# Kernel optimization log

Measured on AMD Instinct MI355X. Metric: run time of the kernel, lower is better.

The kernel has to match this reference:

```python
import jax, jax.numpy as jnp
import numpy as np

R_MAX = 5.0
NUM_BASIS = 8
CUTOFF_P = 6
N_LAYERS = 3
C = 64          # hidden_mul / channels of irreps_conv_out (64x0e+64x1o)
Z = 4           # element_number
AVG_DEG = 32.0  # num-neighbor normalization (E/N)
SQRT3 = 1.7320508075688772
SQRT2 = 1.4142135623730951


def _radial_embedding(r):
    # Bessel basis * polynomial cutoff (RadialEdgeEmbedding)
    rs = jnp.maximum(r, 1e-9)
    n = jnp.arange(1, NUM_BASIS + 1, dtype=r.dtype)  # (B,)
    bessel = jnp.sqrt(2.0 / R_MAX) * jnp.sin(n * jnp.pi * rs[:, None] / R_MAX) / rs[:, None]
    x = r / R_MAX
    p = float(CUTOFF_P)
    fc = (1.0
          - (p + 1.0) * (p + 2.0) / 2.0 * x ** CUTOFF_P
          + p * (p + 2.0) * x ** (CUTOFF_P + 1)
          - p * (p + 1.0) / 2.0 * x ** (CUTOFF_P + 2))
    fc = jnp.where(x < 1.0, fc, 0.0)
    return bessel * fc[:, None]  # (E, NUM_BASIS)


def setup_inputs() -> dict:
    key = jax.random.key(0)
    ks = jax.random.split(key, 20)
    N, E, B = 16000, 512000, 16
    atom_type = jax.random.randint(ks[0], (N,), 0, Z)
    # atoms in a 4A box so most edge lengths fall inside r_max=5
    atom_pos = jax.random.uniform(ks[1], (N, 3), dtype=jnp.float32) * 4.0
    edge_src = jax.random.randint(ks[2], (E,), 0, N)
    edge_dst = jax.random.randint(ks[3], (E,), 0, N)
    edge_cell_shift = jnp.zeros((E, 3), jnp.float32)
    cell = jnp.tile(jnp.eye(3, dtype=jnp.float32) * 10.0, (B, 1, 1)) \
        + 0.01 * jax.random.normal(ks[4], (B, 3, 3), jnp.float32)
    image_index = jax.random.randint(ks[5], (N,), 0, B)
    g = lambda k, s, fan: jax.random.normal(k, s, jnp.float32) / np.sqrt(fan)
    return {
        'atom_type': atom_type, 'atom_pos': atom_pos,
        'edge_src': edge_src, 'edge_dst': edge_dst,
        'edge_cell_shift': edge_cell_shift, 'cell': cell, 'image_index': image_index,
        'w_lin_in': g(ks[6], (Z, C), Z),
        'mlp_w1': g(ks[7], (N_LAYERS, NUM_BASIS, 64), NUM_BASIS),
        'mlp_b1': jnp.zeros((N_LAYERS, 64), jnp.float32),
        'mlp_w2': g(ks[8], (N_LAYERS, 64, 5 * C), 64),
        'w_self_s': g(ks[9], (N_LAYERS, C, C), C),
        'w_self_v': g(ks[10], (N_LAYERS, C, C), C),
        'w_gate': g(ks[11], (N_LAYERS, C, C), C),
        'w_lin1': g(ks[12], (C, 16), C),
        'w_lin2': g(ks[13], (16, 1), 16),
    }


def reference(atom_type, atom_pos, edge_src, edge_dst, edge_cell_shift, cell,
              image_index, w_lin_in, mlp_w1, mlp_b1, mlp_w2,
              w_self_s, w_self_v, w_gate, w_lin1, w_lin2):
    N = atom_pos.shape[0]
    # edge vectors with periodic cell shift
    edge_vec = atom_pos[edge_dst] - atom_pos[edge_src]
    edge_vec = edge_vec + jnp.einsum('ni,nij->nj', edge_cell_shift,
                                     cell.reshape(-1, 3, 3)[image_index[edge_src]])
    r = jnp.linalg.norm(edge_vec, axis=1)                      # (E,)
    unit = edge_vec / jnp.maximum(r, 1e-9)[:, None]
    # spherical harmonics lmax=1, component normalization: y0=1 (implicit), y1=sqrt(3)*unit
    y1 = SQRT3 * unit                                           # (E, 3)
    emb = _radial_embedding(r)                                  # (E, NUM_BASIS)

    # one-hot embedding + input linear (one-hot is all 0e -> scalar channels only)
    onehot = jax.nn.one_hot(atom_type, Z, dtype=atom_pos.dtype)
    s = onehot @ w_lin_in                                       # (N, C) l=0 features
    v = jnp.zeros((N, C, 3), atom_pos.dtype)                    # (N, C, 3) l=1 features

    inv_sqrt_deg = 1.0 / np.sqrt(AVG_DEG)
    for L in range(N_LAYERS):
        # radial MLP -> per-edge per-channel tensor-product path weights
        w = jax.nn.silu(emb @ mlp_w1[L] + mlp_b1[L]) @ mlp_w2[L]  # (E, 5C)
        w1, w2, w3, w4, w5 = jnp.split(w, 5, axis=1)              # (E, C) each
        s_src = s[edge_src]                                       # (E, C)
        v_src = v[edge_src]                                       # (E, C, 3)
        vdoty = jnp.einsum('ecx,ex->ec', v_src, y1)
        # CG tensor-product paths (l<=1):
        m_s = w1 * s_src + w2 * vdoty / SQRT3                     # 0x0->0, 1x1->0
        m_v = (w3[:, :, None] * s_src[:, :, None] * y1[:, None, :]      # 0x1->1
               + w4[:, :, None] * v_src                                  # 1x0->1
               + w5[:, :, None] * jnp.cross(v_src, y1[:, None, :]) / SQRT2)  # 1x1->1
        agg_s = jax.ops.segment_sum(m_s, edge_dst, num_segments=N) * inv_sqrt_deg
        agg_v = jax.ops.segment_sum(m_v, edge_dst, num_segments=N) * inv_sqrt_deg
        # gated self-interaction + resnet
        gate = jax.nn.sigmoid(agg_s @ w_gate[L])                  # (N, C)
        s = s + jax.nn.silu(agg_s @ w_self_s[L])
        v = v + jnp.einsum('ncx,cd->ndx', agg_v, w_self_v[L]) * gate[:, :, None]

    # o3.Linear to 16x0e then 1x0e (only scalar channels map to 0e outputs)
    atomic_energy = (s @ w_lin1) @ w_lin2                         # (N, 1)
    atomic_energy = atomic_energy * 1.0                           # atomic_scale
    return atomic_energy
```

## Files before the change

kernel.cpp:

```cpp
#include <hip/hip_runtime.h>
#include <hip/hip_fp16.h>
#include <math.h>

#define NUM_BASIS 8
#define SQRT3 1.7320508075688772f
#define SQRT2 1.4142135623730951f
#define INV_SQRT_DEG 0.17677669529663687f
#define PI_F 3.14159265358979323846f

typedef _Float16 half8 __attribute__((ext_vector_type(8)));
typedef float float4v __attribute__((ext_vector_type(4)));

__device__ __forceinline__ float sigmoidf_(float x) { return 1.0f / (1.0f + __expf(-x)); }
__device__ __forceinline__ float siluf_(float x) { return x * sigmoidf_(x); }

__device__ __forceinline__ void unp2(unsigned u, float& a, float& b) {
    __half2 h = *reinterpret_cast<__half2*>(&u);
    float2 f = __half22float2(h);
    a = f.x; b = f.y;
}
__device__ __forceinline__ unsigned pk2(float a, float b) {
    __half2 h = __floats2half2_rn(a, b);
    return *reinterpret_cast<unsigned*>(&h);
}

__global__ __launch_bounds__(256) void count_deg(
    const int* __restrict__ dst, int* __restrict__ deg, int E)
{
    int base = (blockIdx.x * blockDim.x + threadIdx.x) * 4;
    if (base + 3 < E) {
        int4 d4 = *(const int4*)(dst + base);
        atomicAdd(&deg[d4.x], 1);
        atomicAdd(&deg[d4.y], 1);
        atomicAdd(&deg[d4.z], 1);
        atomicAdd(&deg[d4.w], 1);
    } else {
        for (int e = base; e < E; e++) atomicAdd(&deg[dst[e]], 1);
    }
}

__global__ __launch_bounds__(1024) void scan_deg(
    const int* __restrict__ deg, int* __restrict__ cursor, int N)
{
    __shared__ int wsum[16];
    __shared__ int carry_s, tot_s;
    int tid = threadIdx.x;
    int wid = tid >> 6, lane = tid & 63;
    if (tid == 0) carry_s = 0;
    __syncthreads();
    for (int base = 0; base < N; base += 16384) {
        int i0 = base + tid * 16;
        int v[16];
        int sum = 0;
        #pragma unroll
        for (int k = 0; k < 16; k++) {
            int i = i0 + k;
            v[k] = (i < N) ? deg[i] : 0;
            sum += v[k];
        }
        int incl = sum;
        #pragma unroll
        for (int off = 1; off < 64; off <<= 1) {
            int t = __shfl_up(incl, off);
            if (lane >= off) incl += t;
        }
        if (lane == 63) wsum[wid] = incl;
        __syncthreads();
        if (wid == 0 && lane < 16) {
            int wv = wsum[lane];
            int wincl = wv;
            #pragma unroll
            for (int off = 1; off < 16; off <<= 1) {
                int t = __shfl_up(wincl, off);
                if (lane >= off) wincl += t;
            }
            wsum[lane] = wincl - wv;
            if (lane == 15) tot_s = wincl;
        }
        __syncthreads();
        int carry = carry_s;
        int run = carry + wsum[wid] + incl - sum;
        #pragma unroll
        for (int k = 0; k < 16; k++) {
            int i = i0 + k;
            if (i < N) cursor[i] = run;
            run += v[k];
        }
        __syncthreads();
        if (tid == 0) carry_s = carry + tot_s;
        __syncthreads();
    }
}

__global__ __launch_bounds__(256) void edge_pre_scatter(
    const float* __restrict__ pos, const int* __restrict__ src,
    const int* __restrict__ dst, const float* __restrict__ cs,
    const float* __restrict__ cell, const int* __restrict__ img,
    int* __restrict__ cursor, _Float16* __restrict__ emb,
    uint2* __restrict__ y14, int2* __restrict__ sdp, int E)
{
    int e = blockIdx.x * blockDim.x + threadIdx.x;
    if (e >= E) return;
    int si = src[e], di = dst[e];
    int slot = atomicAdd(&cursor[di], 1);
    sdp[slot] = make_int2(si, di);
    float vx = pos[di*3+0] - pos[si*3+0];
    float vy = pos[di*3+1] - pos[si*3+1];
    float vz = pos[di*3+2] - pos[si*3+2];
    float c0 = cs[(size_t)e*3+0], c1 = cs[(size_t)e*3+1], c2 = cs[(size_t)e*3+2];
    const float* M = cell + (size_t)img[si] * 9;
    vx += c0*M[0] + c1*M[3] + c2*M[6];
    vy += c0*M[1] + c1*M[4] + c2*M[7];
    vz += c0*M[2] + c1*M[5] + c2*M[8];
    float r  = sqrtf(vx*vx + vy*vy + vz*vz);
    float rs = fmaxf(r, 1e-9f);
    float inv = 1.0f / rs;
    uint2 yv;
    yv.x = pk2(SQRT3*vx*inv, SQRT3*vy*inv);
    yv.y = pk2(SQRT3*vz*inv, 0.f);
    y14[slot] = yv;
    float x = r * (1.0f / 5.0f);
    float x2 = x*x, x6 = x2*x2*x2;
    float fc = 1.0f - 28.0f*x6 + 48.0f*x6*x - 21.0f*x6*x2;
    if (x >= 1.0f) fc = 0.0f;
    float pre = sqrtf(2.0f / 5.0f) * inv * fc;
    float t = PI_F * rs * (1.0f / 5.0f);
    half8 ev;
    #pragma unroll
    for (int n = 1; n <= NUM_BASIS; n++)
        ev[n-1] = (_Float16)(pre * __sinf((float)n * t));
    *(half8*)(emb + (size_t)slot*NUM_BASIS) = ev;
}

__global__ __launch_bounds__(256) void prep_weights(
    const float* __restrict__ W2, _Float16* __restrict__ w2f,
    const float* __restrict__ Wg, const float* __restrict__ Ws,
    const float* __restrict__ Wv, _Float16* __restrict__ wgtf,
    const float* __restrict__ Wl1, const float* __restrict__ Wl2,
    float* __restrict__ wl12)
{
    int idx = blockIdx.x * blockDim.x + threadIdx.x;
    if (idx < 64) {
        float a = 0.f;
        #pragma unroll
        for (int j = 0; j < 16; j++) a = fmaf(Wl1[idx*16 + j], Wl2[j], a);
        wl12[idx] = a;
    }
    if (idx < 3 * 20480) {
        int L  = idx / 20480;
        int r  = idx % 20480;
        int cg = r / 5120;
        int r2 = r % 5120;
        int p  = r2 / 1024;
        int r3 = r2 % 1024;
        int kh = r3 / 512;
        int r4 = r3 % 512;
        int lane = r4 / 8;
        int j  = r4 % 8;
        int k = kh*32 + (lane >> 4)*8 + j;
        int n = p*64 + cg*16 + (lane & 15);
        w2f[idx] = (_Float16)W2[(size_t)L*20480 + k*320 + n];
    } else if (idx < 3*20480 + 3*3*4096) {
        int idx2 = idx - 3*20480;
        int L   = idx2 / 12288;
        int rem = idx2 % 12288;
        int mat = rem / 4096;
        int r2  = rem % 4096;
        int cg  = r2 / 1024;
        int r3  = r2 % 1024;
        int kh  = r3 / 512;
        int r4  = r3 % 512;
        int lane = r4 / 8;
        int j   = r4 % 8;
        int k = kh*32 + (lane >> 4)*8 + j;
        int n = cg*16 + (lane & 15);
        const float* src = (mat == 0) ? Wg : (mat == 1) ? Ws : Wv;
        wgtf[idx2] = (_Float16)src[(size_t)L*4096 + k*64 + n];
    }
}

__device__ __forceinline__ void mlp1_afrag(
    const _Float16* __restrict__ emb, const float* __restrict__ W1,
    const float* __restrict__ B1, int eA, int q, half8 afrag[2])
{
    half8 ev = *(const half8*)(emb + (size_t)eA*8);
    float em[8];
    #pragma unroll
    for (int j = 0; j < 8; j++) em[j] = (float)ev[j];
    #pragma unroll
    for (int kh = 0; kh < 2; kh++) {
        int kb = kh*32 + q*8;
        float hv[8];
        float4 b0 = *(const float4*)(B1 + kb);
        float4 b1 = *(const float4*)(B1 + kb + 4);
        hv[0]=b0.x; hv[1]=b0.y; hv[2]=b0.z; hv[3]=b0.w;
        hv[4]=b1.x; hv[5]=b1.y; hv[6]=b1.z; hv[7]=b1.w;
        #pragma unroll
        for (int jj = 0; jj < 8; jj++) {
            float4 wa = *(const float4*)(W1 + jj*64 + kb);
            float4 wb = *(const float4*)(W1 + jj*64 + kb + 4);
            hv[0] = fmaf(em[jj], wa.x, hv[0]);
            hv[1] = fmaf(em[jj], wa.y, hv[1]);
            hv[2] = fmaf(em[jj], wa.z, hv[2]);
            hv[3] = fmaf(em[jj], wa.w, hv[3]);
            hv[4] = fmaf(em[jj], wb.x, hv[4]);
            hv[5] = fmaf(em[jj], wb.y, hv[5]);
            hv[6] = fmaf(em[jj], wb.z, hv[6]);
            hv[7] = fmaf(em[jj], wb.w, hv[7]);
        }
        #pragma unroll
        for (int j = 0; j < 8; j++)
            afrag[kh][j] = (_Float16)siluf_(hv[j]);
    }
}

__global__ __launch_bounds__(256) void edge_msg_mfma_l0(
    const _Float16* __restrict__ emb, const uint2* __restrict__ y14,
    const int2* __restrict__ sdp,
    const int* __restrict__ type, const float* __restrict__ wlin,
    const float* __restrict__ W1, const float* __restrict__ B1,
    const _Float16* __restrict__ w2f,
    float* __restrict__ aggs, float* __restrict__ aggx,
    float* __restrict__ aggy, float* __restrict__ aggz, int E)
{
    __shared__ _Float16 w2s[20480];
    {
        half8* dstv = (half8*)w2s;
        const half8* srcv = (const half8*)w2f;
        #pragma unroll
        for (int k = 0; k < 10; k++)
            dstv[threadIdx.x + k*256] = srcv[threadIdx.x + k*256];
    }
    __syncthreads();

    int wave  = (blockIdx.x * blockDim.x + threadIdx.x) >> 6;
    int lane  = threadIdx.x & 63;
    int wbase = wave * 16;
    if (wbase >= E) return;
    int q   = lane >> 4;
    int col = lane & 15;

    int eb = wbase + q*4;
    int d[4], tt[4];
    float y1x[4], y1y[4], y1z[4];
    #pragma unroll
    for (int r = 0; r < 4; r++) {
        int2 sv = sdp[eb + r];
        tt[r] = type[sv.x];
        d[r]  = sv.y;
        uint2 yv = y14[eb + r];
        float dummy;
        unp2(yv.x, y1x[r], y1y[r]);
        unp2(yv.y, y1z[r], dummy);
    }

    half8 afrag[2];
    mlp1_afrag(emb, W1, B1, wbase + col, q, afrag);

    int dnq = __shfl_down(d[0], 16);
    int nd3 = (q == 3) ? -1 : dnq;
    int df = d[0], dl = d[3];
    bool U = (df == dl);
    int dlp = __shfl_up(dl, 16);
    bool link = (q > 0) && (dlp == df);

    #pragma unroll
    for (int cg = 0; cg < 4; cg++) {
        float4v a1 = {0,0,0,0}, a3 = {0,0,0,0};
        const _Float16* wbp = w2s + ((size_t)cg*5*2*64*8) + (size_t)lane*8;
        {
            half8 b10 = *(const half8*)(wbp + ((size_t)(0*2 + 0))*64*8);
            half8 b11 = *(const half8*)(wbp + ((size_t)(0*2 + 1))*64*8);
            half8 b30 = *(const half8*)(wbp + ((size_t)(2*2 + 0))*64*8);
            half8 b31 = *(const half8*)(wbp + ((size_t)(2*2 + 1))*64*8);
            a1 = __builtin_amdgcn_mfma_f32_16x16x32_f16(afrag[0], b10, a1, 0, 0, 0);
            a1 = __builtin_amdgcn_mfma_f32_16x16x32_f16(afrag[1], b11, a1, 0, 0, 0);
            a3 = __builtin_amdgcn_mfma_f32_16x16x32_f16(afrag[0], b30, a3, 0, 0, 0);
            a3 = __builtin_amdgcn_mfma_f32_16x16x32_f16(afrag[1], b31, a3, 0, 0, 0);
        }
        int c = cg*16 + col;

        float ms[4], mx[4], my[4], mz[4];
        #pragma unroll
        for (int r = 0; r < 4; r++) {
            float s = wlin[tt[r]*64 + c];
            float w3s = a3[r] * s;
            ms[r] = a1[r] * s;
            mx[r] = w3s * y1x[r];
            my[r] = w3s * y1y[r];
            mz[r] = w3s * y1z[r];
        }
        #pragma unroll
        for (int r = 1; r < 4; r++) {
            if (d[r] == d[r-1]) {
                ms[r] += ms[r-1]; mx[r] += mx[r-1];
                my[r] += my[r-1]; mz[r] += mz[r-1];
            }
        }
        float Cs = 0.f, Cx = 0.f, Cy = 0.f, Cz = 0.f;
        #pragma unroll
        for (int it = 0; it < 3; it++) {
            float es = ms[3] + (U ? Cs : 0.f);
            float ex = mx[3] + (U ? Cx : 0.f);
            float ey = my[3] + (U ? Cy : 0.f);
            float ez = mz[3] + (U ? Cz : 0.f);
            float ts = __shfl_up(es, 16);
            float tx = __shfl_up(ex, 16);
            float ty = __shfl_up(ey, 16);
            float tz = __shfl_up(ez, 16);
            Cs = link ? ts : 0.f; Cx = link ? tx : 0.f;
            Cy = link ? ty : 0.f; Cz = link ? tz : 0.f;
        }
        bool hr = true;
        #pragma unroll
        for (int r = 0; r < 4; r++) {
            if (r > 0) hr = hr && (d[r] == d[r-1]);
            float fs = ms[r] + (hr ? Cs : 0.f);
            float fx = mx[r] + (hr ? Cx : 0.f);
            float fy = my[r] + (hr ? Cy : 0.f);
            float fz = mz[r] + (hr ? Cz : 0.f);
            int ndx = (r < 3) ? d[r+1] : nd3;
            if (ndx != d[r] && d[r] >= 0) {
                size_t ai = (size_t)d[r]*64 + c;
                atomicAdd(aggs + ai, fs);
                atomicAdd(aggx + ai, fx);
                atomicAdd(aggy + ai, fy);
                atomicAdd(aggz + ai, fz);
            }
        }
    }
}

__global__ __launch_bounds__(256) void edge_msg_mfma(
    const _Float16* __restrict__ emb, const uint2* __restrict__ y14,
    const int2* __restrict__ sdp,
    const uint2* __restrict__ nf,
    const float* __restrict__ W1, const float* __restrict__ B1,
    const _Float16* __restrict__ w2f,
    float* __restrict__ aggs, float* __restrict__ aggx,
    float* __restrict__ aggy, float* __restrict__ aggz, int E)
{
    __shared__ _Float16 w2s[20480];
    {
        half8* dstv = (half8*)w2s;
        const half8* srcv = (const half8*)w2f;
        #pragma unroll
        for (int k = 0; k < 10; k++)
            dstv[threadIdx.x + k*256] = srcv[threadIdx.x + k*256];
    }
    __syncthreads();

    int wave  = (blockIdx.x * blockDim.x + threadIdx.x) >> 6;
    int lane  = threadIdx.x & 63;
    int wbase = wave * 16;
    if (wbase >= E) return;
    int q   = lane >> 4;
    int col = lane & 15;

    int eb = wbase + q*4;
    int d[4], si[4];
    float y1x[4], y1y[4], y1z[4];
    #pragma unroll
    for (int r = 0; r < 4; r++) {
        int2 sv = sdp[eb + r];
        si[r] = sv.x;
        d[r]  = sv.y;
        uint2 yv = y14[eb + r];
        float dummy;
        unp2(yv.x, y1x[r], y1y[r]);
        unp2(yv.y, y1z[r], dummy);
    }

    uint2 pf[4][4];
    #pragma unroll
    for (int r = 0; r < 4; r++) {
        size_t nb = (size_t)si[r] * 64 + col;
        pf[r][0] = nf[nb];
        pf[r][1] = nf[nb + 16];
        pf[r][2] = nf[nb + 32];
        pf[r][3] = nf[nb + 48];
    }

    half8 afrag[2];
    mlp1_afrag(emb, W1, B1, wbase + col, q, afrag);

    int dnq = __shfl_down(d[0], 16);
    int nd3 = (q == 3) ? -1 : dnq;
    int df = d[0], dl = d[3];
    bool U = (df == dl);
    int dlp = __shfl_up(dl, 16);
    bool link = (q > 0) && (dlp == df);

    #pragma unroll
    for (int cg = 0; cg < 4; cg++) {
        float4v acc[5];
        #pragma unroll
        for (int p = 0; p < 5; p++) acc[p] = (float4v){0.f, 0.f, 0.f, 0.f};
        const _Float16* wbp = w2s + ((size_t)cg*5*2*64*8) + (size_t)lane*8;
        #pragma unroll
        for (int p = 0; p < 5; p++) {
            half8 bf0 = *(const half8*)(wbp + ((size_t)(p*2 + 0))*64*8);
            half8 bf1 = *(const half8*)(wbp + ((size_t)(p*2 + 1))*64*8);
            acc[p] = __builtin_amdgcn_mfma_f32_16x16x32_f16(afrag[0], bf0, acc[p], 0, 0, 0);
            acc[p] = __builtin_amdgcn_mfma_f32_16x16x32_f16(afrag[1], bf1, acc[p], 0, 0, 0);
        }
        int c = cg*16 + col;

        float ms[4], mx[4], my[4], mz[4];
        #pragma unroll
        for (int r = 0; r < 4; r++) {
            float fsx, fvx, fvy, fvz;
            unp2(pf[r][cg].x, fsx, fvx);
            unp2(pf[r][cg].y, fvy, fvz);
            float yx = y1x[r], yy = y1y[r], yz = y1z[r];
            float w1 = acc[0][r], w2 = acc[1][r], w3 = acc[2][r];
            float w4 = acc[3][r], w5 = acc[4][r];
            float vdoty = fvx*yx + fvy*yy + fvz*yz;
            ms[r] = w1*fsx + w2*vdoty*(1.0f/SQRT3);
            float cx = fvy*yz - fvz*yy;
            float cy = fvz*yx - fvx*yz;
            float cz = fvx*yy - fvy*yx;
            mx[r] = w3*fsx*yx + w4*fvx + w5*cx*(1.0f/SQRT2);
            my[r] = w3*fsx*yy + w4*fvy + w5*cy*(1.0f/SQRT2);
            mz[r] = w3*fsx*yz + w4*fvz + w5*cz*(1.0f/SQRT2);
        }
        #pragma unroll
        for (int r = 1; r < 4; r++) {
            if (d[r] == d[r-1]) {
                ms[r] += ms[r-1]; mx[r] += mx[r-1];
                my[r] += my[r-1]; mz[r] += mz[r-1];
            }
        }
        float Cs = 0.f, Cx = 0.f, Cy = 0.f, Cz = 0.f;
        #pragma unroll
        for (int it = 0; it < 3; it++) {
            float es = ms[3] + (U ? Cs : 0.f);
            float ex = mx[3] + (U ? Cx : 0.f);
            float ey = my[3] + (U ? Cy : 0.f);
            float ez = mz[3] + (U ? Cz : 0.f);
            float ts = __shfl_up(es, 16);
            float tx = __shfl_up(ex, 16);
            float ty = __shfl_up(ey, 16);
            float tz = __shfl_up(ez, 16);
            Cs = link ? ts : 0.f; Cx = link ? tx : 0.f;
            Cy = link ? ty : 0.f; Cz = link ? tz : 0.f;
        }
        bool hr = true;
        #pragma unroll
        for (int r = 0; r < 4; r++) {
            if (r > 0) hr = hr && (d[r] == d[r-1]);
            float fs = ms[r] + (hr ? Cs : 0.f);
            float fx = mx[r] + (hr ? Cx : 0.f);
            float fy = my[r] + (hr ? Cy : 0.f);
            float fz = mz[r] + (hr ? Cz : 0.f);
            int ndx = (r < 3) ? d[r+1] : nd3;
            if (ndx != d[r] && d[r] >= 0) {
                size_t ai = (size_t)d[r]*64 + c;
                atomicAdd(aggs + ai, fs);
                atomicAdd(aggx + ai, fx);
                atomicAdd(aggy + ai, fy);
                atomicAdd(aggz + ai, fz);
            }
        }
    }
}

__global__ __launch_bounds__(256) void node_update_mfma(
    uint2* __restrict__ nf,
    float* __restrict__ aggs, float* __restrict__ aggx,
    float* __restrict__ aggy, float* __restrict__ aggz,
    const _Float16* __restrict__ wgtf,
    const int* __restrict__ type, const float* __restrict__ wlin,
    const float* __restrict__ wl12,
    float* __restrict__ out, int first, int do_out, int N)
{
    __shared__ _Float16 wgs[12288];
    {
        half8* dstv = (half8*)wgs;
        const half8* srcv = (const half8*)wgtf;
        #pragma unroll
        for (int k = 0; k < 6; k++)
            dstv[threadIdx.x + k*256] = srcv[threadIdx.x + k*256];
    }

    int wave  = (blockIdx.x * blockDim.x + threadIdx.x) >> 6;
    int lane  = threadIdx.x & 63;
    int wbase = wave * 16;
    bool active = wbase < N;
    int q = lane >> 4, col = lane & 15;

    int nodeA = active ? (wbase + col) : 0;
    if (nodeA >= N) nodeA = N - 1;
    size_t nb = (size_t)nodeA * 64 + q * 8;
    half8 af0[2], af1[2], af2[2], af3[2];
    #pragma unroll
    for (int kh = 0; kh < 2; kh++) {
        const float* p0 = aggs + nb + kh*32;
        const float* p1 = aggx + nb + kh*32;
        const float* p2 = aggy + nb + kh*32;
        const float* p3 = aggz + nb + kh*32;
        float4 a0 = *(const float4*)p0, b0 = *(const float4*)(p0+4);
        float4 a1 = *(const float4*)p1, b1 = *(const float4*)(p1+4);
        float4 a2 = *(const float4*)p2, b2 = *(const float4*)(p2+4);
        float4 a3 = *(const float4*)p3, b3 = *(const float4*)(p3+4);
        af0[kh][0]=(_Float16)(a0.x*INV_SQRT_DEG); af0[kh][1]=(_Float16)(a0.y*INV_SQRT_DEG);
        af0[kh][2]=(_Float16)(a0.z*INV_SQRT_DEG); af0[kh][3]=(_Float16)(a0.w*INV_SQRT_DEG);
        af0[kh][4]=(_Float16)(b0.x*INV_SQRT_DEG); af0[kh][5]=(_Float16)(b0.y*INV_SQRT_DEG);
        af0[kh][6]=(_Float16)(b0.z*INV_SQRT_DEG); af0[kh][7]=(_Float16)(b0.w*INV_SQRT_DEG);
        af1[kh][0]=(_Float16)(a1.x*INV_SQRT_DEG); af1[kh][1]=(_Float16)(a1.y*INV_SQRT_DEG);
        af1[kh][2]=(_Float16)(a1.z*INV_SQRT_DEG); af1[kh][3]=(_Float16)(a1.w*INV_SQRT_DEG);
        af1[kh][4]=(_Float16)(b1.x*INV_SQRT_DEG); af1[kh][5]=(_Float16)(b1.y*INV_SQRT_DEG);
        af1[kh][6]=(_Float16)(b1.z*INV_SQRT_DEG); af1[kh][7]=(_Float16)(b1.w*INV_SQRT_DEG);
        af2[kh][0]=(_Float16)(a2.x*INV_SQRT_DEG); af2[kh][1]=(_Float16)(a2.y*INV_SQRT_DEG);
        af2[kh][2]=(_Float16)(a2.z*INV_SQRT_DEG); af2[kh][3]=(_Float16)(a2.w*INV_SQRT_DEG);
        af2[kh][4]=(_Float16)(b2.x*INV_SQRT_DEG); af2[kh][5]=(_Float16)(b2.y*INV_SQRT_DEG);
        af2[kh][6]=(_Float16)(b2.z*INV_SQRT_DEG); af2[kh][7]=(_Float16)(b2.w*INV_SQRT_DEG);
        af3[kh][0]=(_Float16)(a3.x*INV_SQRT_DEG); af3[kh][1]=(_Float16)(a3.y*INV_SQRT_DEG);
        af3[kh][2]=(_Float16)(a3.z*INV_SQRT_DEG); af3[kh][3]=(_Float16)(a3.w*INV_SQRT_DEG);
        af3[kh][4]=(_Float16)(b3.x*INV_SQRT_DEG); af3[kh][5]=(_Float16)(b3.y*INV_SQRT_DEG);
        af3[kh][6]=(_Float16)(b3.z*INV_SQRT_DEG); af3[kh][7]=(_Float16)(b3.w*INV_SQRT_DEG);
    }

    int tt[4];
    #pragma unroll
    for (int r = 0; r < 4; r++) {
        int nd = wbase + q*4 + r;
        tt[r] = type[(active && nd < N) ? nd : 0];
    }

    __syncthreads();

    float epart[4] = {0.f, 0.f, 0.f, 0.f};

    #pragma unroll
    for (int cg = 0; cg < 4; cg++) {
        const _Float16* bp = wgs + (size_t)lane * 8;
        half8 bg0 = *(const half8*)(bp + ((size_t)((0*4 + cg)*2 + 0))*512);
        half8 bg1 = *(const half8*)(bp + ((size_t)((0*4 + cg)*2 + 1))*512);
        half8 bs0 = *(const half8*)(bp + ((size_t)((1*4 + cg)*2 + 0))*512);
        half8 bs1 = *(const half8*)(bp + ((size_t)((1*4 + cg)*2 + 1))*512);
        half8 bv0 = *(const half8*)(bp + ((size_t)((2*4 + cg)*2 + 0))*512);
        half8 bv1 = *(const half8*)(bp + ((size_t)((2*4 + cg)*2 + 1))*512);
        float4v ag = {0,0,0,0}, as = {0,0,0,0};
        float4v ox = {0,0,0,0}, oy = {0,0,0,0}, oz = {0,0,0,0};
        ag = __builtin_amdgcn_mfma_f32_16x16x32_f16(af0[0], bg0, ag, 0, 0, 0);
        ag = __builtin_amdgcn_mfma_f32_16x16x32_f16(af0[1], bg1, ag, 0, 0, 0);
        as = __builtin_amdgcn_mfma_f32_16x16x32_f16(af0[0], bs0, as, 0, 0, 0);
        as = __builtin_amdgcn_mfma_f32_16x16x32_f16(af0[1], bs1, as, 0, 0, 0);
        ox = __builtin_amdgcn_mfma_f32_16x16x32_f16(af1[0], bv0, ox, 0, 0, 0);
        ox = __builtin_amdgcn_mfma_f32_16x16x32_f16(af1[1], bv1, ox, 0, 0, 0);
        oy = __builtin_amdgcn_mfma_f32_16x16x32_f16(af2[0], bv0, oy, 0, 0, 0);
        oy = __builtin_amdgcn_mfma_f32_16x16x32_f16(af2[1], bv1, oy, 0, 0, 0);
        oz = __builtin_amdgcn_mfma_f32_16x16x32_f16(af3[0], bv0, oz, 0, 0, 0);
        oz = __builtin_amdgcn_mfma_f32_16x16x32_f16(af3[1], bv1, oz, 0, 0, 0);

        if (!active) continue;
        int c = cg*16 + col;
        float wlc = wl12[c];
        #pragma unroll
        for (int r = 0; r < 4; r++) {
            int nd = wbase + q*4 + r;
            bool wr = nd < N;
            size_t ni = (size_t)nd*64 + c;
            float sx, vx, vy, vz;
            if (first) {
                sx = wlin[tt[r]*64 + c];
                vx = 0.f; vy = 0.f; vz = 0.f;
            } else {
                uint2 cur = nf[wr ? ni : 0];
                unp2(cur.x, sx, vx);
                unp2(cur.y, vy, vz);
            }
            float gate = sigmoidf_(ag[r]);
            sx += siluf_(as[r]);
            vx += ox[r] * gate;
            vy += oy[r] * gate;
            vz += oz[r] * gate;
            if (wr) {
                uint2 nv;
                nv.x = pk2(sx, vx);
                nv.y = pk2(vy, vz);
                nf[ni] = nv;
                aggs[ni] = 0.f;
                aggx[ni] = 0.f;
                aggy[ni] = 0.f;
                aggz[ni] = 0.f;
                epart[r] = fmaf(sx, wlc, epart[r]);
            }
        }
    }
    if (do_out && active) {
        #pragma unroll
        for (int r = 0; r < 4; r++) {
            float e = epart[r];
            e += __shfl_xor(e, 1);
            e += __shfl_xor(e, 2);
            e += __shfl_xor(e, 4);
            e += __shfl_xor(e, 8);
            int nd = wbase + q*4 + r;
            if (col == 0 && nd < N) out[nd] = e;
        }
    }
}

extern "C" void kernel_launch(void* const* d_in, const int* in_sizes, int n_in,
                              void* d_out, int out_size, void* d_ws, size_t ws_size,
                              hipStream_t stream)
{
    const int*   atom_type = (const int*)  d_in[0];
    const float* pos       = (const float*)d_in[1];
    const int*   src       = (const int*)  d_in[2];
    const int*   dst       = (const int*)  d_in[3];
    const float* cs        = (const float*)d_in[4];
    const float* cell      = (const float*)d_in[5];
    const int*   img       = (const int*)  d_in[6];
    const float* wlin_in   = (const float*)d_in[7];
    const float* mw1       = (const float*)d_in[8];
    const float* mb1       = (const float*)d_in[9];
    const float* mw2       = (const float*)d_in[10];
    const float* wss       = (const float*)d_in[11];
    const float* wsv       = (const float*)d_in[12];
    const float* wg        = (const float*)d_in[13];
    const float* wl1       = (const float*)d_in[14];
    const float* wl2       = (const float*)d_in[15];
    int N = in_sizes[0];
    int E = in_sizes[2];

    char* w = (char*)d_ws;
    _Float16* emb = (_Float16*)w; w += (size_t)E * 8 * sizeof(_Float16);
    uint2*  y14  = (uint2*)w;  w += (size_t)E * sizeof(uint2);
    int2*   sdp  = (int2*)w;   w += (size_t)E * sizeof(int2);
    uint2*  nf   = (uint2*)w;  w += (size_t)N * 64 * sizeof(uint2);
    float*  agg  = (float*)w;  w += (size_t)N * 64 * 4 * sizeof(float);
    _Float16* w2f  = (_Float16*)w; w += (size_t)3 * 20480 * sizeof(_Float16);
    _Float16* wgtf = (_Float16*)w; w += (size_t)3 * 3 * 4096 * sizeof(_Float16);
    float*  wl12 = (float*)w;  w += 64 * sizeof(float);
    int*    deg  = (int*)w;    w += (size_t)N * sizeof(int);
    int*    curs = (int*)w;    w += (size_t)N * sizeof(int);

    size_t NC = (size_t)N * 64;
    float* aggs = agg;
    float* aggx = agg + NC;
    float* aggy = agg + 2*NC;
    float* aggz = agg + 3*NC;

    hipMemsetAsync(deg, 0, (size_t)N * sizeof(int), stream);
    hipMemsetAsync(agg, 0, NC * 4 * sizeof(float), stream);
    count_deg<<<(E/4 + 255) / 256, 256, 0, stream>>>(dst, deg, E);
    scan_deg<<<1, 1024, 0, stream>>>(deg, curs, N);
    int prep_n = 3*20480 + 3*3*4096;
    prep_weights<<<(prep_n + 255) / 256, 256, 0, stream>>>(
        mw2, w2f, wg, wss, wsv, wgtf, wl1, wl2, wl12);
    edge_pre_scatter<<<(E + 255) / 256, 256, 0, stream>>>(
        pos, src, dst, cs, cell, img, curs, emb, y14, sdp, E);

    int eblocks = (E + 63) / 64;
    int nblocks = (N + 63) / 64;

    edge_msg_mfma_l0<<<eblocks, 256, 0, stream>>>(
        emb, y14, sdp, atom_type, wlin_in,
        mw1, mb1, w2f, aggs, aggx, aggy, aggz, E);
    node_update_mfma<<<nblocks, 256, 0, stream>>>(
        nf, aggs, aggx, aggy, aggz, wgtf, atom_type, wlin_in, wl12,
        (float*)d_out, 1, 0, N);

    for (int L = 1; L < 3; L++) {
        edge_msg_mfma<<<eblocks, 256, 0, stream>>>(
            emb, y14, sdp, nf,
            mw1 + L * 8 * 64, mb1 + L * 64, w2f + (size_t)L * 20480,
            aggs, aggx, aggy, aggz, E);
        node_update_mfma<<<nblocks, 256, 0, stream>>>(
            nf, aggs, aggx, aggy, aggz,
            wgtf + (size_t)L * 12288, atom_type, wlin_in, wl12,
            (float*)d_out, 0, (L == 2) ? 1 : 0, N);
    }
}
```

Baseline: 482.6 us.

## Split edge-message channels across block pairs and shrink shared weight staging

The layer-0 edge kernel now stages only the two weight paths it actually uses (w1 and w3) in shared memory, cutting LDS from 40KB to 16KB. The general edge kernel splits the 64 channels into two halves handled by paired blocks, so each block stages half the weights (20KB) and holds half the node-feature registers. Launch bounds request 8 blocks per CU to raise occupancy. In exchange, layers 1-2 launch twice as many blocks, which recompute the radial MLP first layer and reload edge metadata redundantly.

```diff
diff --git a/kernel.cpp b/kernel.cpp
--- a/kernel.cpp
+++ b/kernel.cpp
@@ -214,7 +214,7 @@
     }
 }
 
-__global__ __launch_bounds__(256) void edge_msg_mfma_l0(
+__global__ __launch_bounds__(256, 8) void edge_msg_mfma_l0(
     const _Float16* __restrict__ emb, const uint2* __restrict__ y14,
     const int2* __restrict__ sdp,
     const int* __restrict__ type, const float* __restrict__ wlin,
@@ -223,13 +223,19 @@
     float* __restrict__ aggs, float* __restrict__ aggx,
     float* __restrict__ aggy, float* __restrict__ aggz, int E)
 {
-    __shared__ _Float16 w2s[20480];
+    __shared__ _Float16 w2s[8192];
     {
         half8* dstv = (half8*)w2s;
         const half8* srcv = (const half8*)w2f;
         #pragma unroll
-        for (int k = 0; k < 10; k++)
-            dstv[threadIdx.x + k*256] = srcv[threadIdx.x + k*256];
+        for (int k = 0; k < 4; k++) {
+            int t  = threadIdx.x + k*256;
+            int cg = t >> 8;
+            int r  = t & 255;
+            int pp = r >> 7;
+            int rk = r & 127;
+            dstv[t] = srcv[cg*640 + pp*256 + rk];
+        }
     }
     __syncthreads();
 
@@ -267,12 +273,12 @@
     #pragma unroll
     for (int cg = 0; cg < 4; cg++) {
         float4v a1 = {0,0,0,0}, a3 = {0,0,0,0};
-        const _Float16* wbp = w2s + ((size_t)cg*5*2*64*8) + (size_t)lane*8;
+        const _Float16* wbp = w2s + ((size_t)cg*2048) + (size_t)lane*8;
         {
-            half8 b10 = *(const half8*)(wbp + ((size_t)(0*2 + 0))*64*8);
-            half8 b11 = *(const half8*)(wbp + ((size_t)(0*2 + 1))*64*8);
-            half8 b30 = *(const half8*)(wbp + ((size_t)(2*2 + 0))*64*8);
-            half8 b31 = *(const half8*)(wbp + ((size_t)(2*2 + 1))*64*8);
+            half8 b10 = *(const half8*)(wbp + 0*512);
+            half8 b11 = *(const half8*)(wbp + 1*512);
+            half8 b30 = *(const half8*)(wbp + 2*512);
+            half8 b31 = *(const half8*)(wbp + 3*512);
             a1 = __builtin_amdgcn_mfma_f32_16x16x32_f16(afrag[0], b10, a1, 0, 0, 0);
             a1 = __builtin_amdgcn_mfma_f32_16x16x32_f16(afrag[1], b11, a1, 0, 0, 0);
             a3 = __builtin_amdgcn_mfma_f32_16x16x32_f16(afrag[0], b30, a3, 0, 0, 0);
@@ -331,7 +337,7 @@
     }
 }
 
-__global__ __launch_bounds__(256) void edge_msg_mfma(
+__global__ __launch_bounds__(256, 8) void edge_msg_mfma(
     const _Float16* __restrict__ emb, const uint2* __restrict__ y14,
     const int2* __restrict__ sdp,
     const uint2* __restrict__ nf,
@@ -340,17 +346,18 @@
     float* __restrict__ aggs, float* __restrict__ aggx,
     float* __restrict__ aggy, float* __restrict__ aggz, int E)
 {
-    __shared__ _Float16 w2s[20480];
+    __shared__ _Float16 w2s[10240];
+    int cgh = blockIdx.x & 1;
     {
         half8* dstv = (half8*)w2s;
-        const half8* srcv = (const half8*)w2f;
-        #pragma unroll
-        for (int k = 0; k < 10; k++)
+        const half8* srcv = (const half8*)w2f + (size_t)cgh*1280;
+        #pragma unroll
+        for (int k = 0; k < 5; k++)
             dstv[threadIdx.x + k*256] = srcv[threadIdx.x + k*256];
     }
     __syncthreads();
 
-    int wave  = (blockIdx.x * blockDim.x + threadIdx.x) >> 6;
+    int wave  = ((blockIdx.x >> 1) << 2) + (threadIdx.x >> 6);
     int lane  = threadIdx.x & 63;
     int wbase = wave * 16;
     if (wbase >= E) return;
@@ -371,14 +378,12 @@
         unp2(yv.y, y1z[r], dummy);
     }
 
-    uint2 pf[4][4];
+    uint2 pf[4][2];
     #pragma unroll
     for (int r = 0; r < 4; r++) {
-        size_t nb = (size_t)si[r] * 64 + col;
+        size_t nb = (size_t)si[r] * 64 + cgh*32 + col;
         pf[r][0] = nf[nb];
         pf[r][1] = nf[nb + 16];
-        pf[r][2] = nf[nb + 32];
-        pf[r][3] = nf[nb + 48];
     }
 
     half8 afrag[2];
@@ -392,26 +397,26 @@
     bool link = (q > 0) && (dlp == df);
 
     #pragma unroll
-    for (int cg = 0; cg < 4; cg++) {
+    for (int cgl = 0; cgl < 2; cgl++) {
         float4v acc[5];
         #pragma unroll
         for (int p = 0; p < 5; p++) acc[p] = (float4v){0.f, 0.f, 0.f, 0.f};
-        const _Float16* wbp = w2s + ((size_t)cg*5*2*64*8) + (size_t)lane*8;
+        const _Float16* wbp = w2s + ((size_t)cgl*5120) + (size_t)lane*8;
         #pragma unroll
         for (int p = 0; p < 5; p++) {
-            half8 bf0 = *(const half8*)(wbp + ((size_t)(p*2 + 0))*64*8);
-            half8 bf1 = *(const half8*)(wbp + ((size_t)(p*2 + 1))*64*8);
+            half8 bf0 = *(const half8*)(wbp + ((size_t)(p*2 + 0))*512);
+            half8 bf1 = *(const half8*)(wbp + ((size_t)(p*2 + 1))*512);
             acc[p] = __builtin_amdgcn_mfma_f32_16x16x32_f16(afrag[0], bf0, acc[p], 0, 0, 0);
             acc[p] = __builtin_amdgcn_mfma_f32_16x16x32_f16(afrag[1], bf1, acc[p], 0, 0, 0);
         }
-        int c = cg*16 + col;
+        int c = (cgh*2 + cgl)*16 + col;
 
         float ms[4], mx[4], my[4], mz[4];
         #pragma unroll
         for (int r = 0; r < 4; r++) {
             float fsx, fvx, fvy, fvz;
-            unp2(pf[r][cg].x, fsx, fvx);
-            unp2(pf[r][cg].y, fvy, fvz);
+            unp2(pf[r][cgl].x, fsx, fvx);
+            unp2(pf[r][cgl].y, fvy, fvz);
             float yx = y1x[r], yy = y1y[r], yz = y1z[r];
             float w1 = acc[0][r], w2 = acc[1][r], w3 = acc[2][r];
             float w4 = acc[3][r], w5 = acc[4][r];
@@ -665,7 +670,7 @@
         (float*)d_out, 1, 0, N);
 
     for (int L = 1; L < 3; L++) {
-        edge_msg_mfma<<<eblocks, 256, 0, stream>>>(
+        edge_msg_mfma<<<eblocks * 2, 256, 0, stream>>>(
             emb, y14, sdp, nf,
             mw1 + L * 8 * 64, mb1 + L * 64, w2f + (size_t)L * 20480,
             aggs, aggx, aggy, aggz, E);
```

After: 912.1 us. +89.0%, slower.
